# Kernel optimization log

Hardware: AMD Instinct MI355X
Metric: run time of the kernel (lower is better)

The kernel has to match this reference:

```python
import jax, jax.numpy as jnp
import numpy as np

B, L, HID, H, DH = 1, 2048, 1024, 16, 64
KW = 2  # d_conv
EPS = float(np.finfo(np.float32).eps)  # torch RMSNorm eps=None -> dtype eps


def _causal_dw_conv(x, w, b):
    # x: (B, L, D), w: (D, K), b: (D,). Depthwise causal conv, no activation.
    Bs, Ls, D = x.shape
    K = w.shape[1]
    xp = jnp.pad(x, ((0, 0), (K - 1, 0), (0, 0)))
    out = b
    for k in range(K):
        out = out + xp[:, k:k + Ls, :] * w[:, k]
    return out


def setup_inputs() -> dict:
    key = jax.random.key(0)
    ks = jax.random.split(key, 14)
    hidden_states = jax.random.normal(ks[0], (B, L, HID), jnp.float32)
    # masked_fill(attention_mask != 0, -inf): True above diagonal (future masked)
    attention_mask = jnp.triu(jnp.ones((L, L), dtype=bool), 1)[None, None]
    all_dim = 3 * H * DH  # q_size + 2*kv_size with KVH == H
    qkv_w = jax.random.normal(ks[1], (all_dim, HID), jnp.float32) * 0.02
    q_conv_w = jax.random.normal(ks[2], (H * DH, KW), jnp.float32) * 0.5
    q_conv_b = jax.random.normal(ks[3], (H * DH,), jnp.float32) * 0.02
    k_conv_w = jax.random.normal(ks[4], (H * DH, KW), jnp.float32) * 0.5
    k_conv_b = jax.random.normal(ks[5], (H * DH,), jnp.float32) * 0.02
    v_conv_w = jax.random.normal(ks[6], (H * DH, KW), jnp.float32) * 0.5
    v_conv_b = jax.random.normal(ks[7], (H * DH,), jnp.float32) * 0.02
    norm_w = jnp.ones((DH,), jnp.float32)
    A_log = jnp.log(jax.random.uniform(ks[8], (H,), jnp.float32, 1.0, 16.0))
    dt0 = jnp.exp(jax.random.uniform(ks[9], (H,), jnp.float32)
                  * (np.log(0.1) - np.log(0.001)) + np.log(0.001))
    dt0 = jnp.clip(dt0, 1e-4)
    dt_bias = dt0 + jnp.log(-jnp.expm1(-dt0))  # inverse softplus init
    dt_proj_w = jax.random.normal(ks[10], (H, HID), jnp.float32) * 0.02
    dt_proj_b = jnp.zeros((H,), jnp.float32)
    o_w = jax.random.normal(ks[11], (HID, H * DH), jnp.float32) * 0.02
    order_coeff = jnp.ones((1, H, 1, 1), jnp.float32)  # 1/cumprod(arange(1,2))
    return dict(hidden_states=hidden_states, attention_mask=attention_mask,
                qkv_w=qkv_w, q_conv_w=q_conv_w, q_conv_b=q_conv_b,
                k_conv_w=k_conv_w, k_conv_b=k_conv_b, v_conv_w=v_conv_w,
                v_conv_b=v_conv_b, norm_w=norm_w, A_log=A_log, dt_bias=dt_bias,
                dt_proj_w=dt_proj_w, dt_proj_b=dt_proj_b, o_w=o_w,
                order_coeff=order_coeff)


def reference(hidden_states, attention_mask, qkv_w, q_conv_w, q_conv_b,
              k_conv_w, k_conv_b, v_conv_w, v_conv_b, norm_w, A_log, dt_bias,
              dt_proj_w, dt_proj_b, o_w, order_coeff):
    qs = H * DH
    qkv = hidden_states @ qkv_w.T                    # (B, L, 3*H*DH)
    q = _causal_dw_conv(qkv[..., :qs], q_conv_w, q_conv_b)
    k = _causal_dw_conv(qkv[..., qs:2 * qs], k_conv_w, k_conv_b)
    v = _causal_dw_conv(qkv[..., 2 * qs:], v_conv_w, v_conv_b)
    # split heads -> (B, H, L, DH)
    q = q.reshape(B, L, H, DH).transpose(0, 2, 1, 3)
    k = k.reshape(B, L, H, DH).transpose(0, 2, 1, 3)
    v = v.reshape(B, L, H, DH).transpose(0, 2, 1, 3)
    # SSM-style gate: dt (B, L, H)
    dt = jax.nn.softplus(hidden_states @ dt_proj_w.T + dt_proj_b + dt_bias)
    v = v * jnp.swapaxes(dt, 1, 2)[..., None]        # value scaled by dt
    A = -jnp.exp(A_log)[None, None, :] * dt          # (B, L, H)
    A_cumsum = jnp.swapaxes(jnp.cumsum(A, axis=1), 1, 2)  # (B, H, L)
    diff = A_cumsum[:, :, :, None] - A_cumsum[:, :, None, :]  # (B, H, L, L)
    A_mask = jnp.exp(jnp.where(attention_mask, -jnp.inf, diff))
    # order == 1: Taylor series reduces to a single gated linear term
    scores = jnp.einsum('bhld,bhmd->bhlm', q, k) * A_mask * (1.0 / order_coeff)
    out = scores @ v                                  # (B, H, L, DH)
    # RMSNorm over head_dim
    out = out * jax.lax.rsqrt(jnp.mean(out * out, -1, keepdims=True) + EPS) * norm_w
    out = out.transpose(0, 2, 1, 3).reshape(B, L, H * DH)
    return out @ o_w.T
```

## Files before the change

kernel.cpp:

```cpp
#include <hip/hip_runtime.h>
#include <hip/hip_bf16.h>

#define L_SEQ 2048
#define HIDN  1024
#define NH    16
#define DHD   64
#define QKV_N 3072

typedef float f4 __attribute__((ext_vector_type(4)));
typedef __bf16 bf16x8 __attribute__((ext_vector_type(8)));
typedef _Float16 half8 __attribute__((ext_vector_type(8)));
typedef unsigned int u32x2 __attribute__((ext_vector_type(2)));

union H8 {
  half8 h;
  u32x2 u2[2];
  uint4 u4;
};

__device__ __forceinline__ float b2f(unsigned short u) {
  union { unsigned int i; float f; } c; c.i = ((unsigned int)u) << 16; return c.f;
}
__device__ __forceinline__ unsigned short f2b(float f) {
  union { float f; unsigned int i; } c; c.f = f;
  unsigned int r = c.i + 0x7FFFu + ((c.i >> 16) & 1u);
  return (unsigned short)(r >> 16);
}
__device__ __forceinline__ unsigned short f2h(float f) {
  union { _Float16 h; unsigned short u; } c; c.h = (_Float16)f; return c.u;
}
__device__ __forceinline__ void unpack8(uint4 u, float* f) {
  unsigned int w[4] = {u.x, u.y, u.z, u.w};
#pragma unroll
  for (int i = 0; i < 4; ++i) {
    union { unsigned int i_; float f_; } lo, hi;
    lo.i_ = w[i] << 16;
    hi.i_ = w[i] & 0xffff0000u;
    f[2 * i] = lo.f_; f[2 * i + 1] = hi.f_;
  }
}

__global__ void detect_kernel(const unsigned short* __restrict__ hs, int* flag) {
  __shared__ int cnt;
  if (threadIdx.x == 0) cnt = 0;
  __syncthreads();
  int c = 0;
  for (int i = threadIdx.x; i < 8192; i += 256) {
    unsigned int e = (hs[i] >> 7) & 0xFFu;
    if (e >= 140u) c++;
  }
  atomicAdd(&cnt, c);
  __syncthreads();
  if (threadIdx.x == 0) *flag = (cnt >= 32) ? 1 : 0;
}

__global__ __launch_bounds__(256) void convert_big(const void* __restrict__ in,
                                                   unsigned short* __restrict__ out,
                                                   int n, const int* __restrict__ flag) {
  const int i = (blockIdx.x * 256 + threadIdx.x) * 4;
  if (i >= n) return;
  if (*flag) {
    f4 v = *(const f4*)((const float*)in + i);
    ushort4 o;
    o.x = f2b(v[0]); o.y = f2b(v[1]); o.z = f2b(v[2]); o.w = f2b(v[3]);
    *(ushort4*)(out + i) = o;
  } else {
    *(uint2*)(out + i) = *(const uint2*)((const unsigned short*)in + i);
  }
}

__global__ __launch_bounds__(256) void convert_small(
    const void* qw, const void* qb, const void* kw, const void* kb,
    const void* vw, const void* vb, const void* nw, const void* al,
    const void* dtb, const void* dpb, const void* oc,
    float* __restrict__ out, const int* __restrict__ flag) {
  const int f = *flag;
  const void* ptrs[11] = {qw, qb, kw, kb, vw, vb, nw, al, dtb, dpb, oc};
  const int sizes[11] = {2048, 1024, 2048, 1024, 2048, 1024, 64, 16, 16, 16, 16};
  int off = 0;
  for (int a = 0; a < 11; ++a) {
    for (int i = threadIdx.x + blockIdx.x * 256; i < sizes[a]; i += gridDim.x * 256)
      out[off + i] = f ? ((const float*)ptrs[a])[i] : b2f(((const unsigned short*)ptrs[a])[i]);
    off += sizes[a];
  }
}

template <int MODE>
__global__ __launch_bounds__(256) void gemm_bt(
    const unsigned short* __restrict__ A, const unsigned short* __restrict__ B,
    void* __restrict__ Cv, int M, int N, int K, const int* __restrict__ flag)
{
  __shared__ __align__(16) short As[64 * 40];
  __shared__ __align__(16) short Bs[64 * 40];
  const int t = threadIdx.x;
  const int wave = t >> 6, lane = t & 63;
  const int quad = lane >> 4, l16 = lane & 15;
  const int m0 = blockIdx.y * 64, n0 = blockIdx.x * 64;
  const int srow = t >> 2, scol = (t & 3) * 8;
  f4 acc[4];
#pragma unroll
  for (int i = 0; i < 4; ++i) acc[i] = (f4){0.f, 0.f, 0.f, 0.f};
  const unsigned short* ap = A + (size_t)(m0 + srow) * K + scol;
  const unsigned short* bp = B + (size_t)(n0 + srow) * K + scol;
  for (int k0 = 0; k0 < K; k0 += 32) {
    uint4 av = *(const uint4*)(ap + k0);
    uint4 bv = *(const uint4*)(bp + k0);
    __syncthreads();
    *(uint4*)&As[srow * 40 + scol] = av;
    *(uint4*)&Bs[srow * 40 + scol] = bv;
    __syncthreads();
    bf16x8 af = *(const bf16x8*)&As[(wave * 16 + l16) * 40 + quad * 8];
#pragma unroll
    for (int nt = 0; nt < 4; ++nt) {
      bf16x8 bf = *(const bf16x8*)&Bs[(nt * 16 + l16) * 40 + quad * 8];
      acc[nt] = __builtin_amdgcn_mfma_f32_16x16x32_bf16(af, bf, acc[nt], 0, 0, 0);
    }
  }
  const int outf32 = (MODE == 0) ? 1 : (*flag ? 1 : 0);
#pragma unroll
  for (int nt = 0; nt < 4; ++nt) {
#pragma unroll
    for (int r = 0; r < 4; ++r) {
      int m = m0 + wave * 16 + quad * 4 + r;
      int n = n0 + nt * 16 + l16;
      if (outf32) ((float*)Cv)[(size_t)m * N + n] = acc[nt][r];
      else        ((unsigned short*)Cv)[(size_t)m * N + n] = f2b(acc[nt][r]);
    }
  }
}

__global__ __launch_bounds__(256) void dt_kernel(
    const unsigned short* __restrict__ hs,
    const unsigned short* __restrict__ dtw,
    const float* __restrict__ smallf,
    float* __restrict__ dt_out, float* __restrict__ A_out)
{
  const int l = blockIdx.x;
  const int t = threadIdx.x, wave = t >> 6, lane = t & 63;
  const unsigned short* hp = hs + (size_t)l * HIDN + lane * 16;
  float hv[16];
  unpack8(*(const uint4*)hp, hv);
  unpack8(*(const uint4*)(hp + 8), hv + 8);
#pragma unroll
  for (int hh = 0; hh < 4; ++hh) {
    const int hd = wave * 4 + hh;
    const unsigned short* wp = dtw + (size_t)hd * HIDN + lane * 16;
    float wv[16];
    unpack8(*(const uint4*)wp, wv);
    unpack8(*(const uint4*)(wp + 8), wv + 8);
    float p = 0.f;
#pragma unroll
    for (int i = 0; i < 16; ++i) p += hv[i] * wv[i];
#pragma unroll
    for (int off = 32; off > 0; off >>= 1) p += __shfl_down(p, off);
    if (lane == 0) {
      float z = p + smallf[9312 + hd] + smallf[9296 + hd];
      float dtv = (z > 20.f) ? z : log1pf(expf(z));
      dt_out[l * NH + hd] = dtv;
      A_out[l * NH + hd] = -expf(smallf[9280 + hd]) * dtv;
    }
  }
}

__global__ __launch_bounds__(64) void cumsum_kernel(const float* __restrict__ A_in,
                                                    float* __restrict__ Ac)
{
  const int h = blockIdx.x;
  const int lane = threadIdx.x;
  const int base = lane * 32;
  float run = 0.f;
  for (int i = 0; i < 32; ++i) run += A_in[(base + i) * NH + h];
  float incl = run;
#pragma unroll
  for (int off = 1; off < 64; off <<= 1) {
    float n = __shfl_up(incl, off);
    if (lane >= off) incl += n;
  }
  float r2 = incl - run;
  for (int i = 0; i < 32; ++i) {
    r2 += A_in[(base + i) * NH + h];
    Ac[h * L_SEQ + base + i] = r2;
  }
}

__global__ __launch_bounds__(256) void conv_kernel(
    const float* __restrict__ qkv, const float* __restrict__ smallf,
    const float* __restrict__ dt, unsigned short* __restrict__ qc)
{
  const int idx = blockIdx.x * 256 + threadIdx.x;
  const int l = idx / (QKV_N / 4);
  const int c = (idx % (QKV_N / 4)) * 4;
  f4 xc = *(const f4*)&qkv[(size_t)l * QKV_N + c];
  f4 xp = (f4){0.f, 0.f, 0.f, 0.f};
  if (l > 0) xp = *(const f4*)&qkv[(size_t)(l - 1) * QKV_N + c];
  const float* w; const float* b; int cb;
  if (c < HIDN)          { w = smallf;        b = smallf + 2048; cb = c; }
  else if (c < 2 * HIDN) { w = smallf + 3072; b = smallf + 5120; cb = c - HIDN; }
  else                   { w = smallf + 6144; b = smallf + 8192; cb = c - 2 * HIDN; }
  f4 o;
#pragma unroll
  for (int j = 0; j < 4; ++j)
    o[j] = b[cb + j] + xp[j] * w[(cb + j) * 2] + xc[j] * w[(cb + j) * 2 + 1];
  if (c >= 2 * HIDN) {
    const int hh = (c - 2 * HIDN) >> 6;
    o *= dt[l * NH + hh];
  }
  ushort4 st;
  st.x = f2h(o[0]); st.y = f2h(o[1]); st.z = f2h(o[2]); st.w = f2h(o[3]);
  *(ushort4*)&qc[(size_t)l * QKV_N + c] = st;
}

__global__ __launch_bounds__(256) void transpose_v(
    const unsigned short* __restrict__ qc, unsigned short* __restrict__ vt)
{
  const int h = blockIdx.y;
  const int l0 = blockIdx.x * 64;
  const int t = threadIdx.x;
  const int srow = t >> 2, cc = t & 3;
  __shared__ __align__(16) unsigned short Ts[64 * 68];
  const unsigned short* gp =
      qc + (size_t)(l0 + srow) * QKV_N + 2 * HIDN + h * DHD + cc * 16;
  uint4 a = *(const uint4*)gp;
  uint4 b = *(const uint4*)(gp + 8);
  *(uint4*)&Ts[srow * 68 + cc * 16] = a;
  *(uint4*)&Ts[srow * 68 + cc * 16 + 8] = b;
  __syncthreads();
  __align__(16) unsigned short o[16];
#pragma unroll
  for (int j = 0; j < 16; ++j) o[j] = Ts[(cc * 16 + j) * 68 + srow];
  unsigned short* op = vt + ((size_t)h * DHD + srow) * L_SEQ + l0 + cc * 16;
  *(uint4*)op = *(const uint4*)&o[0];
  *(uint4*)(op + 8) = *(const uint4*)&o[8];
}

__global__ __launch_bounds__(256) void attn_kernel(
    const unsigned short* __restrict__ qc,
    const unsigned short* __restrict__ vt,
    const float* __restrict__ Ac,
    const float* __restrict__ smallf,
    unsigned short* __restrict__ attn_out)
{
  const int h  = blockIdx.y;
  const int lt = 31 - blockIdx.x;
  const int t  = threadIdx.x;
  const int w    = t >> 6;
  const int lane = t & 63;
  const int l16  = lane & 15;
  const int quad = lane >> 4;
  const int srow = t >> 2;
  const int cc   = t & 3;

  __shared__ __align__(16) unsigned short K_lds[2][64 * 68];
  __shared__ __align__(16) unsigned short V_lds[2][64 * 68];
  __shared__ __align__(16) unsigned short S_lds[64 * 68];

  const int l0 = lt * 64;
  const float rc = 1.0f / smallf[9328 + h];
  const float* Acp = Ac + h * L_SEQ;

  H8 qf0, qf1;
  {
    const unsigned short* qp =
        qc + (size_t)(l0 + w * 16 + l16) * QKV_N + h * DHD + quad * 8;
    qf0.u4 = *(const uint4*)qp;
    qf1.u4 = *(const uint4*)(qp + 32);
  }
  float alv[4];
#pragma unroll
  for (int r = 0; r < 4; ++r) alv[r] = Acp[l0 + w * 16 + quad * 4 + r];

  f4 acc[4];
#pragma unroll
  for (int i = 0; i < 4; ++i) acc[i] = (f4){0.f, 0.f, 0.f, 0.f};

  const unsigned short* kgp =
      qc + (size_t)srow * QKV_N + HIDN + h * DHD + cc * 16;
  const unsigned short* vgp =
      vt + ((size_t)h * DHD + srow) * L_SEQ + cc * 16;

  const int swo = srow * 68 + cc * 16;

  uint4 k0v = *(const uint4*)kgp,       k1v = *(const uint4*)(kgp + 8);
  uint4 v0v = *(const uint4*)vgp,       v1v = *(const uint4*)(vgp + 8);

  int cur = 0;
  for (int it = 0; it <= lt; ++it) {
    unsigned short* Kl = K_lds[cur];
    unsigned short* Vl = V_lds[cur];
    *(u32x2*)&Kl[swo]      = (u32x2){k0v.x, k0v.y};
    *(u32x2*)&Kl[swo + 4]  = (u32x2){k0v.z, k0v.w};
    *(u32x2*)&Kl[swo + 8]  = (u32x2){k1v.x, k1v.y};
    *(u32x2*)&Kl[swo + 12] = (u32x2){k1v.z, k1v.w};
    *(u32x2*)&Vl[swo]      = (u32x2){v0v.x, v0v.y};
    *(u32x2*)&Vl[swo + 4]  = (u32x2){v0v.z, v0v.w};
    *(u32x2*)&Vl[swo + 8]  = (u32x2){v1v.x, v1v.y};
    *(u32x2*)&Vl[swo + 12] = (u32x2){v1v.z, v1v.w};
    if (it < lt) {
      const unsigned short* kp = kgp + (size_t)(it + 1) * 64 * QKV_N;
      const unsigned short* vp = vgp + (size_t)(it + 1) * 64;
      k0v = *(const uint4*)kp; k1v = *(const uint4*)(kp + 8);
      v0v = *(const uint4*)vp; v1v = *(const uint4*)(vp + 8);
    }
    __syncthreads();

    f4 s[4];
#pragma unroll
    for (int i = 0; i < 4; ++i) s[i] = (f4){0.f, 0.f, 0.f, 0.f};
#pragma unroll
    for (int ks = 0; ks < 2; ++ks) {
      H8 qk = ks ? qf1 : qf0;
#pragma unroll
      for (int nt = 0; nt < 4; ++nt) {
        H8 kf;
        const int ko = (nt * 16 + l16) * 68 + ks * 32 + quad * 8;
        kf.u2[0] = *(const u32x2*)&K_lds[cur][ko];
        kf.u2[1] = *(const u32x2*)&K_lds[cur][ko + 4];
        s[nt] = __builtin_amdgcn_mfma_f32_16x16x32_f16(qk.h, kf.h, s[nt], 0, 0, 0);
      }
    }
    const int m0 = it * 64;
#pragma unroll
    for (int nt = 0; nt < 4; ++nt) {
      const int mg = m0 + nt * 16 + l16;
      const float am = Acp[mg];
#pragma unroll
      for (int r = 0; r < 4; ++r) {
        const int lg = l0 + w * 16 + quad * 4 + r;
        float val = (mg <= lg) ? s[nt][r] * __expf(alv[r] - am) * rc : 0.0f;
        S_lds[(w * 16 + quad * 4 + r) * 68 + nt * 16 + l16] = f2h(val);
      }
    }
#pragma unroll
    for (int ks = 0; ks < 2; ++ks) {
      H8 sa;
      const int so = (w * 16 + l16) * 68 + ks * 32 + quad * 8;
      sa.u2[0] = *(const u32x2*)&S_lds[so];
      sa.u2[1] = *(const u32x2*)&S_lds[so + 4];
#pragma unroll
      for (int db = 0; db < 4; ++db) {
        H8 vb;
        const int vo = (db * 16 + l16) * 68 + ks * 32 + quad * 8;
        vb.u2[0] = *(const u32x2*)&V_lds[cur][vo];
        vb.u2[1] = *(const u32x2*)&V_lds[cur][vo + 4];
        acc[db] = __builtin_amdgcn_mfma_f32_16x16x32_f16(sa.h, vb.h, acc[db], 0, 0, 0);
      }
    }
    cur ^= 1;
  }

#pragma unroll
  for (int r = 0; r < 4; ++r) {
    float p = acc[0][r] * acc[0][r] + acc[1][r] * acc[1][r]
            + acc[2][r] * acc[2][r] + acc[3][r] * acc[3][r];
#pragma unroll
    for (int off = 1; off < 16; off <<= 1) p += __shfl_xor(p, off);
    const float rn = rsqrtf(p * (1.0f / 64.0f) + 1.1920928955078125e-07f);
    unsigned short* op =
        attn_out + (size_t)(l0 + w * 16 + quad * 4 + r) * HIDN + h * DHD + l16;
#pragma unroll
    for (int ds = 0; ds < 4; ++ds)
      op[ds * 16] = f2b(acc[ds][r] * rn * smallf[9216 + ds * 16 + l16]);
  }
}

extern "C" void kernel_launch(void* const* d_in, const int* in_sizes, int n_in,
                              void* d_out, int out_size, void* d_ws, size_t ws_size,
                              hipStream_t stream)
{
  (void)in_sizes; (void)n_in; (void)out_size; (void)ws_size;
  const void* hs        = d_in[0];
  const void* qkv_w     = d_in[2];
  const void* q_conv_w  = d_in[3];
  const void* q_conv_b  = d_in[4];
  const void* k_conv_w  = d_in[5];
  const void* k_conv_b  = d_in[6];
  const void* v_conv_w  = d_in[7];
  const void* v_conv_b  = d_in[8];
  const void* norm_w    = d_in[9];
  const void* A_log     = d_in[10];
  const void* dt_bias   = d_in[11];
  const void* dt_proj_w = d_in[12];
  const void* dt_proj_b = d_in[13];
  const void* o_w       = d_in[14];
  const void* ordc      = d_in[15];

  char* ws = (char*)d_ws;
  int* flag             = (int*)ws;
  unsigned short* hs_b  = (unsigned short*)(ws + 256);
  unsigned short* qkvw_b= (unsigned short*)(ws + 4194560);
  unsigned short* ow_b  = (unsigned short*)(ws + 10486016);
  unsigned short* dtw_b = (unsigned short*)(ws + 12583168);
  float* smallf         = (float*)(ws + 12615936);
  float* qkv            = (float*)(ws + 12653568);
  unsigned short* qc_h  = (unsigned short*)(ws + 37819392);
  float* dtbuf          = (float*)(ws + 62985216);
  float* Abuf           = (float*)(ws + 63116288);
  float* Acum           = (float*)(ws + 63247360);
  unsigned short* attnb = (unsigned short*)(ws + 63378432);
  unsigned short* vt_h  = (unsigned short*)(ws + 67572736);

  detect_kernel<<<1, 256, 0, stream>>>((const unsigned short*)hs, flag);
  convert_big<<<(2097152 / 4 + 255) / 256, 256, 0, stream>>>(hs, hs_b, 2097152, flag);
  convert_big<<<(3145728 / 4 + 255) / 256, 256, 0, stream>>>(qkv_w, qkvw_b, 3145728, flag);
  convert_big<<<(1048576 / 4 + 255) / 256, 256, 0, stream>>>(o_w, ow_b, 1048576, flag);
  convert_big<<<(16384 / 4 + 255) / 256, 256, 0, stream>>>(dt_proj_w, dtw_b, 16384, flag);
  convert_small<<<4, 256, 0, stream>>>(q_conv_w, q_conv_b, k_conv_w, k_conv_b,
                                       v_conv_w, v_conv_b, norm_w, A_log,
                                       dt_bias, dt_proj_b, ordc, smallf, flag);

  gemm_bt<0><<<dim3(QKV_N / 64, L_SEQ / 64), 256, 0, stream>>>(
      hs_b, qkvw_b, qkv, L_SEQ, QKV_N, HIDN, flag);
  dt_kernel<<<L_SEQ, 256, 0, stream>>>(hs_b, dtw_b, smallf, dtbuf, Abuf);
  cumsum_kernel<<<NH, 64, 0, stream>>>(Abuf, Acum);
  conv_kernel<<<(L_SEQ * QKV_N / 4) / 256, 256, 0, stream>>>(qkv, smallf, dtbuf, qc_h);
  transpose_v<<<dim3(L_SEQ / 64, NH), 256, 0, stream>>>(qc_h, vt_h);
  attn_kernel<<<dim3(32, NH), 256, 0, stream>>>(qc_h, vt_h, Acum, smallf, attnb);
  gemm_bt<1><<<dim3(HIDN / 64, L_SEQ / 64), 256, 0, stream>>>(
      attnb, ow_b, d_out, L_SEQ, HIDN, HIDN, flag);
}
```

Before: 270.7 us.

## Use 128x128 register-prefetched GEMM for QKV projection and balance attention tile order

Adds a new 128x128-tile bf16 MFMA GEMM with register prefetch of the next K-slice and uses it for the QKV projection instead of the 64x64 gemm_bt. Each wave now computes a 64x64 sub-tile, which raises data reuse per LDS load. The launch drops to 384 blocks, which may under-fill the GPU. The attention kernel also reverses tile order for half the heads so heavy and light causal tiles mix across dispatch, aiming at better load balance.

```diff
diff --git a/kernel.cpp b/kernel.cpp
--- a/kernel.cpp
+++ b/kernel.cpp
@@ -85,6 +85,68 @@
   }
 }
 
+__global__ __launch_bounds__(256) void gemm128(
+    const unsigned short* __restrict__ A, const unsigned short* __restrict__ B,
+    float* __restrict__ C, int M, int N, int K)
+{
+  __shared__ __align__(16) unsigned short As[128 * 40];
+  __shared__ __align__(16) unsigned short Bs[128 * 40];
+  const int t = threadIdx.x;
+  const int w = t >> 6, lane = t & 63;
+  const int quad = lane >> 4, l16 = lane & 15;
+  const int wr = w >> 1, wc = w & 1;
+  const int m0 = blockIdx.y * 128, n0 = blockIdx.x * 128;
+  const int srow = t >> 1;
+  const int scol = (t & 1) * 16;
+
+  f4 acc[4][4];
+#pragma unroll
+  for (int i = 0; i < 4; ++i)
+#pragma unroll
+    for (int j = 0; j < 4; ++j) acc[i][j] = (f4){0.f, 0.f, 0.f, 0.f};
+
+  const unsigned short* apg = A + (size_t)(m0 + srow) * K + scol;
+  const unsigned short* bpg = B + (size_t)(n0 + srow) * K + scol;
+  uint4 a0 = *(const uint4*)apg,       a1 = *(const uint4*)(apg + 8);
+  uint4 b0 = *(const uint4*)bpg,       b1 = *(const uint4*)(bpg + 8);
+
+  for (int k0 = 0; k0 < K; k0 += 32) {
+    __syncthreads();
+    *(uint4*)&As[srow * 40 + scol]     = a0;
+    *(uint4*)&As[srow * 40 + scol + 8] = a1;
+    *(uint4*)&Bs[srow * 40 + scol]     = b0;
+    *(uint4*)&Bs[srow * 40 + scol + 8] = b1;
+    __syncthreads();
+    if (k0 + 32 < K) {
+      a0 = *(const uint4*)(apg + k0 + 32); a1 = *(const uint4*)(apg + k0 + 40);
+      b0 = *(const uint4*)(bpg + k0 + 32); b1 = *(const uint4*)(bpg + k0 + 40);
+    }
+    bf16x8 aF[4], bF[4];
+#pragma unroll
+    for (int i = 0; i < 4; ++i)
+      aF[i] = *(const bf16x8*)&As[(wr * 64 + i * 16 + l16) * 40 + quad * 8];
+#pragma unroll
+    for (int j = 0; j < 4; ++j)
+      bF[j] = *(const bf16x8*)&Bs[(wc * 64 + j * 16 + l16) * 40 + quad * 8];
+#pragma unroll
+    for (int i = 0; i < 4; ++i)
+#pragma unroll
+      for (int j = 0; j < 4; ++j)
+        acc[i][j] = __builtin_amdgcn_mfma_f32_16x16x32_bf16(aF[i], bF[j], acc[i][j], 0, 0, 0);
+  }
+
+#pragma unroll
+  for (int i = 0; i < 4; ++i)
+#pragma unroll
+    for (int j = 0; j < 4; ++j)
+#pragma unroll
+      for (int r = 0; r < 4; ++r) {
+        int m = m0 + wr * 64 + i * 16 + quad * 4 + r;
+        int n = n0 + wc * 64 + j * 16 + l16;
+        C[(size_t)m * N + n] = acc[i][j][r];
+      }
+}
+
 template <int MODE>
 __global__ __launch_bounds__(256) void gemm_bt(
     const unsigned short* __restrict__ A, const unsigned short* __restrict__ B,
@@ -241,7 +303,8 @@
     unsigned short* __restrict__ attn_out)
 {
   const int h  = blockIdx.y;
-  const int lt = 31 - blockIdx.x;
+  const int bx = blockIdx.x;
+  const int lt = (h < 8) ? (31 - bx) : bx;
   const int t  = threadIdx.x;
   const int w    = t >> 6;
   const int lane = t & 63;
@@ -408,8 +471,8 @@
                                        v_conv_w, v_conv_b, norm_w, A_log,
                                        dt_bias, dt_proj_b, ordc, smallf, flag);
 
-  gemm_bt<0><<<dim3(QKV_N / 64, L_SEQ / 64), 256, 0, stream>>>(
-      hs_b, qkvw_b, qkv, L_SEQ, QKV_N, HIDN, flag);
+  gemm128<<<dim3(QKV_N / 128, L_SEQ / 128), 256, 0, stream>>>(
+      hs_b, qkvw_b, qkv, L_SEQ, QKV_N, HIDN);
   dt_kernel<<<L_SEQ, 256, 0, stream>>>(hs_b, dtw_b, smallf, dtbuf, Abuf);
   cumsum_kernel<<<NH, 64, 0, stream>>>(Abuf, Acum);
   conv_kernel<<<(L_SEQ * QKV_N / 4) / 256, 256, 0, stream>>>(qkv, smallf, dtbuf, qc_h);
```

After: 257.1 us. 1.05x faster.
